# Performance work log

Measured on AMD Instinct MI355X. Metric: run time of the kernel, lower is better.

## Reference

```python
import jax, jax.numpy as jnp
import numpy as np

H = 128  # h_size


def setup_inputs() -> dict:
    key = jax.random.key(0)
    ks = jax.random.split(key, 6)
    depth, n_trees = 16, 4
    N = 2 ** depth - 1          # nodes per complete binary tree
    T = n_trees * N             # total nodes
    return {
        "iou": jax.random.normal(ks[0], (T, 3 * H), dtype=jnp.float32),
        "h": jax.random.normal(ks[1], (T, H), dtype=jnp.float32),
        "c": jax.random.normal(ks[2], (T, H), dtype=jnp.float32),
        "W_iou": jax.random.normal(ks[3], (3 * H, 2 * H), dtype=jnp.float32) * 0.05,
        "b_iou": jnp.zeros((3 * H,), dtype=jnp.float32),
        "W_f": jax.random.normal(ks[4], (2 * H, 2 * H), dtype=jnp.float32) * 0.05,
        "b_f": jnp.zeros((2 * H,), dtype=jnp.float32),
        "depth": depth,
        "n_trees": n_trees,
    }


def _gates(iou, b_iou):
    i, o, u = jnp.split(iou + b_iou, 3, axis=1)
    return jax.nn.sigmoid(i), jax.nn.sigmoid(o), jnp.tanh(u)


def reference(iou, h, c, W_iou, b_iou, W_f, b_f, depth, n_trees):
    N = 2 ** depth - 1
    offs = (jnp.arange(n_trees) * N)[:, None]  # per-tree node offsets

    # --- leaf frontier: no messages -> apply_node_func only (keeps initial iou, c) ---
    l = depth - 1
    idx = (offs + jnp.arange(2 ** l - 1, 2 ** (l + 1) - 1)[None, :]).reshape(-1)
    i, o, u = _gates(iou[idx], b_iou)
    c_new = i * u + c[idx]
    h = h.at[idx].set(o * jnp.tanh(c_new))
    c = c.at[idx].set(c_new)

    # --- internal levels, bottom-up (level-parallel topological propagation) ---
    for l in range(depth - 2, -1, -1):
        loc = jnp.arange(2 ** l - 1, 2 ** (l + 1) - 1)
        idx = (offs + loc[None, :]).reshape(-1)
        lidx = (offs + (2 * loc + 1)[None, :]).reshape(-1)  # left child
        ridx = lidx + 1                                      # right child
        # reduce_func: gather children, forget gates, sum-reduce c, new iou
        h_cat = jnp.concatenate([h[lidx], h[ridx]], axis=-1)          # [n, 2H]
        f = jax.nn.sigmoid(h_cat @ W_f.T + b_f).reshape(-1, 2, H)     # [n, 2, H]
        c_kids = jnp.stack([c[lidx], c[ridx]], axis=1)                # [n, 2, H]
        c_red = jnp.sum(f * c_kids, axis=1)                           # [n, H]
        iou_red = h_cat @ W_iou.T                                     # [n, 3H]
        # apply_node_func
        i, o, u = _gates(iou_red, b_iou)
        c_new = i * u + c_red
        h = h.at[idx].set(o * jnp.tanh(c_new))
        c = c.at[idx].set(c_new)
    return h
```

## Files before the change

### kernel.cpp

```cpp
#include <hip/hip_runtime.h>

#define HH   128
#define H2   256
#define H3   384
#define NPT  65535
#define MT   32
#define TPB  512

typedef __bf16    bf16x8 __attribute__((ext_vector_type(8)));
typedef float     f32x4  __attribute__((ext_vector_type(4)));
typedef _Float16  f16x4  __attribute__((ext_vector_type(4)));
typedef _Float16  half_t;

__device__ unsigned short Wb_g[640 * 256];

__device__ __forceinline__ float fsig(float x)  { return 1.0f / (1.0f + __expf(-x)); }
__device__ __forceinline__ float ftanh(float x) { return 1.0f - 2.0f / (__expf(2.0f * x) + 1.0f); }
__device__ __forceinline__ unsigned short f2bf(float f) {
    unsigned u = __float_as_uint(f);
    u += 0x7fffu + ((u >> 16) & 1u);
    return (unsigned short)(u >> 16);
}
__device__ __forceinline__ int swz(int off) { return off ^ (((off >> 9) & 7) << 4); }

__global__ __launch_bounds__(256) void conv_k(const float* __restrict__ W_iou,
                                              const float* __restrict__ W_f)
{
    int t    = blockIdx.x * 256 + threadIdx.x;
    int base = t * 4;
    int j = base >> 8, k = base & 255;
    const float* src = (j < H3) ? (W_iou + j * H2 + k)
                                : (W_f + (j - H3) * H2 + k);
    float4 v = *(const float4*)src;
    ushort4 p;
    p.x = f2bf(v.x); p.y = f2bf(v.y); p.z = f2bf(v.z); p.w = f2bf(v.w);
    *(ushort4*)(Wb_g + base) = p;
}

__global__ __launch_bounds__(256) void leaf_k(
    const float* __restrict__ iou, const float* __restrict__ c_in,
    const float* __restrict__ b_iou,
    float* __restrict__ h_out, half_t* __restrict__ c_ws,
    unsigned short* __restrict__ h_bf)
{
    int g    = blockIdx.x * 256 + threadIdx.x;
    int node = g >> 5;
    int e    = (g & 31) << 2;
    int tree = node >> 15;
    int loc  = 32767 + (node & 32767);
    int row  = tree * NPT + loc;

    const float* ip = iou + (size_t)row * H3;
    float4 vi = *(const float4*)(ip + e);
    float4 vo = *(const float4*)(ip + HH + e);
    float4 vu = *(const float4*)(ip + 2 * HH + e);
    float4 vc = *(const float4*)(c_in + row * HH + e);
    float4 bi = *(const float4*)(b_iou + e);
    float4 bo = *(const float4*)(b_iou + HH + e);
    float4 bu = *(const float4*)(b_iou + 2 * HH + e);

    float4 hn, cn;
#define DOL(X) { float iv = fsig(vi.X + bi.X); float ov = fsig(vo.X + bo.X); \
                 float uv = ftanh(vu.X + bu.X); float cv = iv * uv + vc.X;   \
                 cn.X = cv; hn.X = ov * ftanh(cv); }
    DOL(x) DOL(y) DOL(z) DOL(w)
#undef DOL
    *(float4*)(h_out + row * HH + e) = hn;
    f16x4 cf; cf.x = (half_t)cn.x; cf.y = (half_t)cn.y; cf.z = (half_t)cn.z; cf.w = (half_t)cn.w;
    *(f16x4*)(c_ws + row * HH + e) = cf;
    ushort4 hb;
    hb.x = f2bf(hn.x); hb.y = f2bf(hn.y); hb.z = f2bf(hn.z); hb.w = f2bf(hn.w);
    *(ushort4*)(h_bf + row * HH + e) = hb;
}

__device__ __forceinline__ void mfma_from(const unsigned char* tile,
                                          const unsigned short* Wp,
                                          f32x4 acc[2][5], int lr, int lc)
{
#pragma unroll
    for (int kk = 0; kk < 8; ++kk) {
        bf16x8 a0 = *(const bf16x8*)(tile + swz(lr * 512 + kk * 64 + lc * 16));
        bf16x8 a1 = *(const bf16x8*)(tile + swz((16 + lr) * 512 + kk * 64 + lc * 16));
#pragma unroll
        for (int g = 0; g < 5; ++g) {
            bf16x8 b = *(const bf16x8*)(Wp + g * HH * H2 + kk * 32);
            acc[0][g] = __builtin_amdgcn_mfma_f32_16x16x32_bf16(a0, b, acc[0][g], 0, 0, 0);
            acc[1][g] = __builtin_amdgcn_mfma_f32_16x16x32_bf16(a1, b, acc[1][g], 0, 0, 0);
        }
    }
}

#define GATES(AC, MTI, RI, CL, CR, HV, CV) \
    { float pi = AC[MTI][0][RI] + bi, po = AC[MTI][1][RI] + bo, pu = AC[MTI][2][RI] + bu; \
      float pl = AC[MTI][3][RI] + bl, pr = AC[MTI][4][RI] + br;                           \
      CV = fsig(pi) * ftanh(pu) + fsig(pl) * (CL) + fsig(pr) * (CR);                      \
      HV = fsig(po) * ftanh(CV); }

__device__ __forceinline__ void do_tile(
    int lvl, int tile,
    float bi, float bo, float bu, float bl, float br,
    float* __restrict__ h_g, half_t* __restrict__ c_ws,
    unsigned short* __restrict__ h_bf,
    unsigned short* A_lds,
    int tid, int w, int lr, int lc, int ee)
{
    const int node0 = tile * MT;
    const int loc0  = (1 << lvl) - 1;
    const int lmask = loc0;

    __syncthreads();

#pragma unroll
    for (int it = 0; it < 2; ++it) {
        int item = tid + TPB * it;
        int m = item >> 5, u = item & 31;
        int node = node0 + m;
        int tree = node >> lvl;
        int loc  = loc0 + (node & lmask);
        int coff = (tree * NPT + 2 * loc + 1 + (u >> 4)) * HH + (u & 15) * 8;
        uint4 v = *(const uint4*)(h_bf + coff);
        *(uint4*)((char*)A_lds + swz(m * 512 + u * 16)) = v;
    }
    __syncthreads();

    int   rofs[2][4];
    float clv[2][4], crv[2][4];
#pragma unroll
    for (int mt = 0; mt < 2; ++mt)
#pragma unroll
        for (int r = 0; r < 4; ++r) {
            int node = node0 + mt * 16 + lc * 4 + r;
            int tree = node >> lvl;
            int loc  = loc0 + (node & lmask);
            int base = tree * NPT + loc;
            int lrow = base + loc + 1;
            rofs[mt][r] = base * HH + ee;
            clv[mt][r] = (float)c_ws[lrow * HH + ee];
            crv[mt][r] = (float)c_ws[lrow * HH + HH + ee];
        }

    f32x4 acc[2][5] = {};
    const unsigned short* Wp = Wb_g + ee * H2 + lc * 8;
    mfma_from((const unsigned char*)A_lds, Wp, acc, lr, lc);

#pragma unroll
    for (int mt = 0; mt < 2; ++mt)
#pragma unroll
        for (int r = 0; r < 4; ++r) {
            float hv, cv;
            GATES(acc, mt, r, clv[mt][r], crv[mt][r], hv, cv);
            int o = rofs[mt][r];
            h_g[o]  = hv;
            c_ws[o] = (half_t)cv;
            h_bf[o] = f2bf(hv);
        }
}

__global__ __launch_bounds__(TPB, 4) void level_k(
    int lvl,
    const float* __restrict__ b_iou, const float* __restrict__ b_f,
    float* __restrict__ h_g, half_t* __restrict__ c_ws,
    unsigned short* __restrict__ h_bf)
{
    __shared__ __align__(16) unsigned short A_lds[MT * H2];
    const int tid = threadIdx.x;
    const int w = tid >> 6, lr = tid & 15, lc = (tid & 63) >> 4;
    const int ee = w * 16 + lr;
    const float bi = b_iou[ee], bo = b_iou[HH + ee], bu = b_iou[2 * HH + ee];
    const float bl = b_f[ee],   br = b_f[HH + ee];
    do_tile(lvl, blockIdx.x, bi, bo, bu, bl, br, h_g, c_ws, h_bf, A_lds, tid, w, lr, lc, ee);
}

__global__ __launch_bounds__(TPB, 2) void solo_k(
    const float* __restrict__ b_iou, const float* __restrict__ b_f,
    float* __restrict__ h_g, half_t* __restrict__ c_ws,
    const unsigned short* __restrict__ h_bf)
{
    __shared__ __align__(16) unsigned char hb[32768];

    const int tid = threadIdx.x;
    const int w = tid >> 6, lr = tid & 15, lc = (tid & 63) >> 4;
    const int ee = w * 16 + lr;
    const int tb = blockIdx.x * NPT;
    const float bi = b_iou[ee], bo = b_iou[HH + ee], bu = b_iou[2 * HH + ee];
    const float bl = b_f[ee],   br = b_f[HH + ee];

    bf16x8 Bf[5][8];
    const unsigned short* Wp = Wb_g + ee * H2 + lc * 8;
#pragma unroll
    for (int g = 0; g < 5; ++g)
#pragma unroll
        for (int kk = 0; kk < 8; ++kk)
            Bf[g][kk] = *(const bf16x8*)(Wp + g * HH * H2 + kk * 32);

#pragma unroll
    for (int it = 0; it < 2; ++it) {
        int p = tid + TPB * it;
        int cc = p >> 4, q = p & 15;
        uint4 v = *(const uint4*)(h_bf + (tb + 63 + cc) * HH + q * 8);
        *(uint4*)(hb + swz(p * 16)) = v;
    }

#pragma unroll 1
    for (int l = 5; l >= 0; --l) {
        const int nl     = 1 << l;
        const int loc0   = nl - 1;
        const int cloc0  = 2 * nl - 1;
        const int cbase  = (l & 1) ? 0 : 16384;
        const int obase  = cbase ^ 16384;
        const bool mt1   = (nl > 16);

        __syncthreads();

        f32x4 acc[2][5] = {};
#pragma unroll
        for (int kk = 0; kk < 8; ++kk) {
            bf16x8 a0 = *(const bf16x8*)(hb + cbase + swz(lr * 512 + kk * 64 + lc * 16));
#pragma unroll
            for (int g = 0; g < 5; ++g)
                acc[0][g] = __builtin_amdgcn_mfma_f32_16x16x32_bf16(a0, Bf[g][kk], acc[0][g], 0, 0, 0);
            if (mt1) {
                bf16x8 a1 = *(const bf16x8*)(hb + cbase + swz((16 + lr) * 512 + kk * 64 + lc * 16));
#pragma unroll
                for (int g = 0; g < 5; ++g)
                    acc[1][g] = __builtin_amdgcn_mfma_f32_16x16x32_bf16(a1, Bf[g][kk], acc[1][g], 0, 0, 0);
            }
        }
        __syncthreads();

#pragma unroll
        for (int mt = 0; mt < 2; ++mt)
#pragma unroll
            for (int r = 0; r < 4; ++r) {
                int j = mt * 16 + lc * 4 + r;
                if (j >= nl) continue;
                int row  = tb + loc0 + j;
                int lrow = tb + cloc0 + 2 * j;
                float hv, cv;
                GATES(acc, mt, r, (float)c_ws[lrow * HH + ee], (float)c_ws[lrow * HH + HH + ee], hv, cv);
                h_g[row * HH + ee]  = hv;
                c_ws[row * HH + ee] = (half_t)cv;
                *(unsigned short*)(hb + obase + swz(j * 256 + ee * 2)) = f2bf(hv);
            }
    }
}

extern "C" void kernel_launch(void* const* d_in, const int* in_sizes, int n_in,
                              void* d_out, int out_size, void* d_ws, size_t ws_size,
                              hipStream_t stream)
{
    const float* iou   = (const float*)d_in[0];
    const float* c_in  = (const float*)d_in[2];
    const float* W_iou = (const float*)d_in[3];
    const float* b_iou = (const float*)d_in[4];
    const float* W_f   = (const float*)d_in[5];
    const float* b_f   = (const float*)d_in[6];
    float* h_out = (float*)d_out;
    half_t* c_ws = (half_t*)d_ws;
    unsigned short* h_bf = (unsigned short*)((char*)d_ws + (size_t)72 * 1024 * 1024);

    conv_k<<<160, 256, 0, stream>>>(W_iou, W_f);
    leaf_k<<<16384, 256, 0, stream>>>(iou, c_in, b_iou, h_out, c_ws, h_bf);

    for (int l = 14; l >= 6; --l) {
        int blocks = (4 << l) / MT;
        level_k<<<blocks, TPB, 0, stream>>>(l, b_iou, b_f, h_out, c_ws, h_bf);
    }
    solo_k<<<4, TPB, 0, stream>>>(b_iou, b_f, h_out, c_ws, h_bf);
}
```

Baseline: 361.6 us.

## Stage child tiles with async global-to-LDS loads and double-buffer level 14

```diff
diff --git a/kernel.cpp b/kernel.cpp
--- a/kernel.cpp
+++ b/kernel.cpp
@@ -11,6 +11,9 @@
 typedef float     f32x4  __attribute__((ext_vector_type(4)));
 typedef _Float16  f16x4  __attribute__((ext_vector_type(4)));
 typedef _Float16  half_t;
+
+typedef __attribute__((address_space(1))) const unsigned int gref_u32;
+typedef __attribute__((address_space(3))) unsigned int       lref_u32;
 
 __device__ unsigned short Wb_g[640 * 256];
 
@@ -43,7 +46,8 @@
     float* __restrict__ h_out, half_t* __restrict__ c_ws,
     unsigned short* __restrict__ h_bf)
 {
-    int g    = blockIdx.x * 256 + threadIdx.x;
+    int bs   = (blockIdx.x & 7) * 2048 + (blockIdx.x >> 3);
+    int g    = bs * 256 + threadIdx.x;
     int node = g >> 5;
     int e    = (g & 31) << 2;
     int tree = node >> 15;
@@ -96,20 +100,13 @@
       CV = fsig(pi) * ftanh(pu) + fsig(pl) * (CL) + fsig(pr) * (CR);                      \
       HV = fsig(po) * ftanh(CV); }
 
-__device__ __forceinline__ void do_tile(
-    int lvl, int tile,
-    float bi, float bo, float bu, float bl, float br,
-    float* __restrict__ h_g, half_t* __restrict__ c_ws,
-    unsigned short* __restrict__ h_bf,
-    unsigned short* A_lds,
-    int tid, int w, int lr, int lc, int ee)
+__device__ __forceinline__ void stage_tile(
+    int lvl, int tile, const unsigned short* __restrict__ h_bf,
+    unsigned short* A, int tid)
 {
     const int node0 = tile * MT;
     const int loc0  = (1 << lvl) - 1;
     const int lmask = loc0;
-
-    __syncthreads();
-
 #pragma unroll
     for (int it = 0; it < 2; ++it) {
         int item = tid + TPB * it;
@@ -117,11 +114,24 @@
         int node = node0 + m;
         int tree = node >> lvl;
         int loc  = loc0 + (node & lmask);
-        int coff = (tree * NPT + 2 * loc + 1 + (u >> 4)) * HH + (u & 15) * 8;
-        uint4 v = *(const uint4*)(h_bf + coff);
-        *(uint4*)((char*)A_lds + swz(m * 512 + u * 16)) = v;
-    }
-    __syncthreads();
+        int pairE = (tree * NPT + 2 * loc + 1) * HH;
+        int sb    = (u * 16) ^ ((m & 7) << 4);
+        __builtin_amdgcn_global_load_lds(
+            (gref_u32*)((const char*)h_bf + (size_t)pairE * 2 + sb),
+            (lref_u32*)((char*)A + item * 16), 16, 0, 0);
+    }
+}
+
+__device__ __forceinline__ void compute_tile(
+    int lvl, int tile, const unsigned short* A,
+    float bi, float bo, float bu, float bl, float br,
+    float* __restrict__ h_g, half_t* __restrict__ c_ws,
+    unsigned short* __restrict__ h_bf,
+    int lr, int lc, int ee)
+{
+    const int node0 = tile * MT;
+    const int loc0  = (1 << lvl) - 1;
+    const int lmask = loc0;
 
     int   rofs[2][4];
     float clv[2][4], crv[2][4];
@@ -141,7 +151,7 @@
 
     f32x4 acc[2][5] = {};
     const unsigned short* Wp = Wb_g + ee * H2 + lc * 8;
-    mfma_from((const unsigned char*)A_lds, Wp, acc, lr, lc);
+    mfma_from((const unsigned char*)A, Wp, acc, lr, lc);
 
 #pragma unroll
     for (int mt = 0; mt < 2; ++mt)
@@ -157,18 +167,32 @@
 }
 
 __global__ __launch_bounds__(TPB, 4) void level_k(
-    int lvl,
+    int lvl, int tpb_t,
     const float* __restrict__ b_iou, const float* __restrict__ b_f,
     float* __restrict__ h_g, half_t* __restrict__ c_ws,
     unsigned short* __restrict__ h_bf)
 {
-    __shared__ __align__(16) unsigned short A_lds[MT * H2];
+    __shared__ __align__(16) unsigned short A_lds[2][MT * H2];
+
     const int tid = threadIdx.x;
     const int w = tid >> 6, lr = tid & 15, lc = (tid & 63) >> 4;
     const int ee = w * 16 + lr;
     const float bi = b_iou[ee], bo = b_iou[HH + ee], bu = b_iou[2 * HH + ee];
     const float bl = b_f[ee],   br = b_f[HH + ee];
-    do_tile(lvl, blockIdx.x, bi, bo, bu, bl, br, h_g, c_ws, h_bf, A_lds, tid, w, lr, lc, ee);
+
+    const int nblk = gridDim.x;
+    const int bs   = (blockIdx.x & 7) * (nblk >> 3) + (blockIdx.x >> 3);
+    const int t0   = bs * tpb_t;
+
+    stage_tile(lvl, t0, h_bf, A_lds[0], tid);
+#pragma unroll 1
+    for (int i = 0; i < tpb_t; ++i) {
+        __syncthreads();
+        if (i + 1 < tpb_t)
+            stage_tile(lvl, t0 + i + 1, h_bf, A_lds[(i + 1) & 1], tid);
+        compute_tile(lvl, t0 + i, A_lds[i & 1],
+                     bi, bo, bu, bl, br, h_g, c_ws, h_bf, lr, lc, ee);
+    }
 }
 
 __global__ __launch_bounds__(TPB, 2) void solo_k(
@@ -262,9 +286,10 @@
     conv_k<<<160, 256, 0, stream>>>(W_iou, W_f);
     leaf_k<<<16384, 256, 0, stream>>>(iou, c_in, b_iou, h_out, c_ws, h_bf);
 
-    for (int l = 14; l >= 6; --l) {
+    level_k<<<1024, TPB, 0, stream>>>(14, 2, b_iou, b_f, h_out, c_ws, h_bf);
+    for (int l = 13; l >= 6; --l) {
         int blocks = (4 << l) / MT;
-        level_k<<<blocks, TPB, 0, stream>>>(l, b_iou, b_f, h_out, c_ws, h_bf);
+        level_k<<<blocks, TPB, 0, stream>>>(l, 1, b_iou, b_f, h_out, c_ws, h_bf);
     }
     solo_k<<<4, TPB, 0, stream>>>(b_iou, b_f, h_out, c_ws, h_bf);
 }
```

Result: slower. 456.0 us (+26.1%).

## Fuse leaf activation with level-14 reduction, keeping leaf state in LDS

Applied to the files above, without the earlier changes.

```diff
diff --git a/kernel.cpp b/kernel.cpp
--- a/kernel.cpp
+++ b/kernel.cpp
@@ -4,7 +4,6 @@
 #define H2   256
 #define H3   384
 #define NPT  65535
-#define MT   32
 #define TPB  512
 
 typedef __bf16    bf16x8 __attribute__((ext_vector_type(8)));
@@ -37,50 +36,68 @@
     *(ushort4*)(Wb_g + base) = p;
 }
 
-__global__ __launch_bounds__(256) void leaf_k(
+#define GATES5(PI, PO, PU, PL, PR, CL, CR, HV, CV) \
+    { CV = fsig(PI) * ftanh(PU) + fsig(PL) * (CL) + fsig(PR) * (CR); \
+      HV = fsig(PO) * ftanh(CV); }
+
+__global__ __launch_bounds__(TPB, 4) void leaf14_k(
     const float* __restrict__ iou, const float* __restrict__ c_in,
-    const float* __restrict__ b_iou,
-    float* __restrict__ h_out, half_t* __restrict__ c_ws,
+    const float* __restrict__ b_iou, const float* __restrict__ b_f,
+    float* __restrict__ h_g, half_t* __restrict__ c_ws,
     unsigned short* __restrict__ h_bf)
 {
-    int g    = blockIdx.x * 256 + threadIdx.x;
-    int node = g >> 5;
-    int e    = (g & 31) << 2;
-    int tree = node >> 15;
-    int loc  = 32767 + (node & 32767);
-    int row  = tree * NPT + loc;
-
-    const float* ip = iou + (size_t)row * H3;
-    float4 vi = *(const float4*)(ip + e);
-    float4 vo = *(const float4*)(ip + HH + e);
-    float4 vu = *(const float4*)(ip + 2 * HH + e);
-    float4 vc = *(const float4*)(c_in + row * HH + e);
-    float4 bi = *(const float4*)(b_iou + e);
-    float4 bo = *(const float4*)(b_iou + HH + e);
-    float4 bu = *(const float4*)(b_iou + 2 * HH + e);
-
-    float4 hn, cn;
+    __shared__ __align__(16) unsigned short A_lds[32 * H2];
+    __shared__ __align__(16) half_t         C_lds[64 * HH];
+
+    const int tid = threadIdx.x;
+    const int w  = tid >> 6;
+    const int lr = tid & 15;
+    const int lc = (tid & 63) >> 4;
+    const int ee = w * 16 + lr;
+    const int node0 = blockIdx.x * 32;
+    const int tree  = node0 >> 14;
+    const int lbase = tree * NPT + 32767 + 2 * (node0 & 16383);
+
+#pragma unroll
+    for (int it = 0; it < 4; ++it) {
+        int p   = tid + TPB * it;
+        int row = p >> 5;
+        int e4  = p & 31;
+        int grow = lbase + row;
+        const float* ip = iou + (size_t)grow * H3 + e4 * 4;
+        float4 vi = *(const float4*)(ip);
+        float4 vo = *(const float4*)(ip + HH);
+        float4 vu = *(const float4*)(ip + 2 * HH);
+        float4 vc = *(const float4*)(c_in + (size_t)grow * HH + e4 * 4);
+        float4 bi = *(const float4*)(b_iou + e4 * 4);
+        float4 bo = *(const float4*)(b_iou + HH + e4 * 4);
+        float4 bu = *(const float4*)(b_iou + 2 * HH + e4 * 4);
+
+        float4 hn, cn;
 #define DOL(X) { float iv = fsig(vi.X + bi.X); float ov = fsig(vo.X + bo.X); \
                  float uv = ftanh(vu.X + bu.X); float cv = iv * uv + vc.X;   \
                  cn.X = cv; hn.X = ov * ftanh(cv); }
-    DOL(x) DOL(y) DOL(z) DOL(w)
+        DOL(x) DOL(y) DOL(z) DOL(w)
 #undef DOL
-    *(float4*)(h_out + row * HH + e) = hn;
-    f16x4 cf; cf.x = (half_t)cn.x; cf.y = (half_t)cn.y; cf.z = (half_t)cn.z; cf.w = (half_t)cn.w;
-    *(f16x4*)(c_ws + row * HH + e) = cf;
-    ushort4 hb;
-    hb.x = f2bf(hn.x); hb.y = f2bf(hn.y); hb.z = f2bf(hn.z); hb.w = f2bf(hn.w);
-    *(ushort4*)(h_bf + row * HH + e) = hb;
-}
-
-__device__ __forceinline__ void mfma_from(const unsigned char* tile,
-                                          const unsigned short* Wp,
-                                          f32x4 acc[2][5], int lr, int lc)
-{
+        *(float4*)(h_g + (size_t)grow * HH + e4 * 4) = hn;
+        f16x4 cf; cf.x = (half_t)cn.x; cf.y = (half_t)cn.y;
+        cf.z = (half_t)cn.z; cf.w = (half_t)cn.w;
+        *(f16x4*)(C_lds + row * HH + e4 * 4) = cf;
+        int m = row >> 1, half = row & 1;
+        uint2 pk;
+        pk.x = (unsigned)f2bf(hn.x) | ((unsigned)f2bf(hn.y) << 16);
+        pk.y = (unsigned)f2bf(hn.z) | ((unsigned)f2bf(hn.w) << 16);
+        int byte = (m * 512 + half * 256 + e4 * 8) ^ ((m & 7) << 4);
+        *(uint2*)((char*)A_lds + byte) = pk;
+    }
+    __syncthreads();
+
+    f32x4 acc[2][5] = {};
+    const unsigned short* Wp = Wb_g + ee * H2 + lc * 8;
 #pragma unroll
     for (int kk = 0; kk < 8; ++kk) {
-        bf16x8 a0 = *(const bf16x8*)(tile + swz(lr * 512 + kk * 64 + lc * 16));
-        bf16x8 a1 = *(const bf16x8*)(tile + swz((16 + lr) * 512 + kk * 64 + lc * 16));
+        bf16x8 a0 = *(const bf16x8*)((const char*)A_lds + swz(lr * 512 + kk * 64 + lc * 16));
+        bf16x8 a1 = *(const bf16x8*)((const char*)A_lds + swz((16 + lr) * 512 + kk * 64 + lc * 16));
 #pragma unroll
         for (int g = 0; g < 5; ++g) {
             bf16x8 b = *(const bf16x8*)(Wp + g * HH * H2 + kk * 32);
@@ -88,27 +105,44 @@
             acc[1][g] = __builtin_amdgcn_mfma_f32_16x16x32_bf16(a1, b, acc[1][g], 0, 0, 0);
         }
     }
-}
-
-#define GATES(AC, MTI, RI, CL, CR, HV, CV) \
-    { float pi = AC[MTI][0][RI] + bi, po = AC[MTI][1][RI] + bo, pu = AC[MTI][2][RI] + bu; \
-      float pl = AC[MTI][3][RI] + bl, pr = AC[MTI][4][RI] + br;                           \
-      CV = fsig(pi) * ftanh(pu) + fsig(pl) * (CL) + fsig(pr) * (CR);                      \
-      HV = fsig(po) * ftanh(CV); }
-
-__device__ __forceinline__ void do_tile(
-    int lvl, int tile,
-    float bi, float bo, float bu, float bl, float br,
+
+    const float bi = b_iou[ee], bo = b_iou[HH + ee], bu = b_iou[2 * HH + ee];
+    const float bl = b_f[ee],   br = b_f[HH + ee];
+#pragma unroll
+    for (int mt = 0; mt < 2; ++mt)
+#pragma unroll
+        for (int r = 0; r < 4; ++r) {
+            int q    = mt * 16 + lc * 4 + r;
+            int node = node0 + q;
+            int base = tree * NPT + 16383 + (node & 16383);
+            int o    = base * HH + ee;
+            float cl = (float)C_lds[(2 * q) * HH + ee];
+            float cr = (float)C_lds[(2 * q + 1) * HH + ee];
+            float hv, cv;
+            GATES5(acc[mt][0][r] + bi, acc[mt][1][r] + bo, acc[mt][2][r] + bu,
+                   acc[mt][3][r] + bl, acc[mt][4][r] + br, cl, cr, hv, cv);
+            h_g[o]  = hv;
+            c_ws[o] = (half_t)cv;
+            h_bf[o] = f2bf(hv);
+        }
+}
+
+__global__ __launch_bounds__(TPB, 4) void level_k(
+    int lvl,
+    const float* __restrict__ b_iou, const float* __restrict__ b_f,
     float* __restrict__ h_g, half_t* __restrict__ c_ws,
-    unsigned short* __restrict__ h_bf,
-    unsigned short* A_lds,
-    int tid, int w, int lr, int lc, int ee)
-{
-    const int node0 = tile * MT;
+    unsigned short* __restrict__ h_bf)
+{
+    __shared__ __align__(16) unsigned short A_lds[32 * H2];
+
+    const int tid = threadIdx.x;
+    const int w  = tid >> 6;
+    const int lr = tid & 15;
+    const int lc = (tid & 63) >> 4;
+    const int ee = w * 16 + lr;
+    const int node0 = blockIdx.x * 32;
     const int loc0  = (1 << lvl) - 1;
     const int lmask = loc0;
-
-    __syncthreads();
 
 #pragma unroll
     for (int it = 0; it < 2; ++it) {
@@ -141,34 +175,32 @@
 
     f32x4 acc[2][5] = {};
     const unsigned short* Wp = Wb_g + ee * H2 + lc * 8;
-    mfma_from((const unsigned char*)A_lds, Wp, acc, lr, lc);
-
+#pragma unroll
+    for (int kk = 0; kk < 8; ++kk) {
+        bf16x8 a0 = *(const bf16x8*)((const char*)A_lds + swz(lr * 512 + kk * 64 + lc * 16));
+        bf16x8 a1 = *(const bf16x8*)((const char*)A_lds + swz((16 + lr) * 512 + kk * 64 + lc * 16));
+#pragma unroll
+        for (int g = 0; g < 5; ++g) {
+            bf16x8 b = *(const bf16x8*)(Wp + g * HH * H2 + kk * 32);
+            acc[0][g] = __builtin_amdgcn_mfma_f32_16x16x32_bf16(a0, b, acc[0][g], 0, 0, 0);
+            acc[1][g] = __builtin_amdgcn_mfma_f32_16x16x32_bf16(a1, b, acc[1][g], 0, 0, 0);
+        }
+    }
+
+    const float bi = b_iou[ee], bo = b_iou[HH + ee], bu = b_iou[2 * HH + ee];
+    const float bl = b_f[ee],   br = b_f[HH + ee];
 #pragma unroll
     for (int mt = 0; mt < 2; ++mt)
 #pragma unroll
         for (int r = 0; r < 4; ++r) {
             float hv, cv;
-            GATES(acc, mt, r, clv[mt][r], crv[mt][r], hv, cv);
+            GATES5(acc[mt][0][r] + bi, acc[mt][1][r] + bo, acc[mt][2][r] + bu,
+                   acc[mt][3][r] + bl, acc[mt][4][r] + br, clv[mt][r], crv[mt][r], hv, cv);
             int o = rofs[mt][r];
             h_g[o]  = hv;
             c_ws[o] = (half_t)cv;
             h_bf[o] = f2bf(hv);
         }
-}
-
-__global__ __launch_bounds__(TPB, 4) void level_k(
-    int lvl,
-    const float* __restrict__ b_iou, const float* __restrict__ b_f,
-    float* __restrict__ h_g, half_t* __restrict__ c_ws,
-    unsigned short* __restrict__ h_bf)
-{
-    __shared__ __align__(16) unsigned short A_lds[MT * H2];
-    const int tid = threadIdx.x;
-    const int w = tid >> 6, lr = tid & 15, lc = (tid & 63) >> 4;
-    const int ee = w * 16 + lr;
-    const float bi = b_iou[ee], bo = b_iou[HH + ee], bu = b_iou[2 * HH + ee];
-    const float bl = b_f[ee],   br = b_f[HH + ee];
-    do_tile(lvl, blockIdx.x, bi, bo, bu, bl, br, h_g, c_ws, h_bf, A_lds, tid, w, lr, lc, ee);
 }
 
 __global__ __launch_bounds__(TPB, 2) void solo_k(
@@ -236,8 +268,11 @@
                 if (j >= nl) continue;
                 int row  = tb + loc0 + j;
                 int lrow = tb + cloc0 + 2 * j;
+                float cl = (float)c_ws[lrow * HH + ee];
+                float cr = (float)c_ws[lrow * HH + HH + ee];
                 float hv, cv;
-                GATES(acc, mt, r, (float)c_ws[lrow * HH + ee], (float)c_ws[lrow * HH + HH + ee], hv, cv);
+                GATES5(acc[mt][0][r] + bi, acc[mt][1][r] + bo, acc[mt][2][r] + bu,
+                       acc[mt][3][r] + bl, acc[mt][4][r] + br, cl, cr, hv, cv);
                 h_g[row * HH + ee]  = hv;
                 c_ws[row * HH + ee] = (half_t)cv;
                 *(unsigned short*)(hb + obase + swz(j * 256 + ee * 2)) = f2bf(hv);
@@ -260,10 +295,9 @@
     unsigned short* h_bf = (unsigned short*)((char*)d_ws + (size_t)72 * 1024 * 1024);
 
     conv_k<<<160, 256, 0, stream>>>(W_iou, W_f);
-    leaf_k<<<16384, 256, 0, stream>>>(iou, c_in, b_iou, h_out, c_ws, h_bf);
-
-    for (int l = 14; l >= 6; --l) {
-        int blocks = (4 << l) / MT;
+    leaf14_k<<<2048, TPB, 0, stream>>>(iou, c_in, b_iou, b_f, h_out, c_ws, h_bf);
+    for (int l = 13; l >= 6; --l) {
+        int blocks = (4 << l) / 32;
         level_k<<<blocks, TPB, 0, stream>>>(l, b_iou, b_f, h_out, c_ws, h_bf);
     }
     solo_k<<<4, TPB, 0, stream>>>(b_iou, b_f, h_out, c_ws, h_bf);
```

Result: faster. 346.7 us (-4.1%).
